# Kernel tuning notes

Hardware: AMD Instinct MI355X
Metric: run time of the kernel (lower is better)

## Reference

```python
import jax, jax.numpy as jnp
import numpy as np

# 4D conv dimension numbers: N=batch, C/I/O=channels, T,Z,Y,X = 4 spatial dims
DN = ('NCTZYX', 'OITZYX', 'NCTZYX')
PAD = [(1, 1)] * 4  # padding=1 on each of the 4 spatial dims


def setup_inputs() -> dict:
    key = jax.random.key(0)
    kx, kw = jax.random.split(key)
    B, Cin, Cout = 1, 16, 4
    T, D, H, Wd = 10, 32, 64, 64
    K = 3
    x = jax.random.normal(kx, (B, Cin, T, D, H, Wd), dtype=jnp.float32)
    # xavier_uniform over [Cout, Cin, 3,3,3,3]
    fan_in = Cin * K ** 4
    fan_out = Cout * K ** 4
    limit = float(np.sqrt(6.0 / (fan_in + fan_out)))
    W = jax.random.uniform(kw, (Cout, Cin, K, K, K, K), dtype=jnp.float32,
                           minval=-limit, maxval=limit)
    b = jnp.zeros((Cout,), dtype=jnp.float32)
    return {"x": x, "W": W, "b": b}


def reference(x, W, b):
    # True 4D convolution (stride 1, padding 1, 'same' output) + channel softmax
    y = jax.lax.conv_general_dilated(
        x, W,
        window_strides=(1, 1, 1, 1),
        padding=PAD,
        dimension_numbers=DN,
    )
    y = y + b[None, :, None, None, None, None]
    return jax.nn.softmax(y, axis=1)
```

## Files before the change

kernel.cpp:

```cpp
#include <hip/hip_runtime.h>
#include <hip/hip_bf16.h>

#define CIN  16
#define COUT 4
#define TT   10
#define ZZ   32
#define YY   64
#define XX   64

constexpr int SX_CI = TT * ZZ * YY * XX;
constexpr int SX_T  = ZZ * YY * XX;
constexpr int SX_Z  = YY * XX;
constexpr int WCO   = CIN * 81;

constexpr int XT_TB = ZZ * YY * XX * CIN * 2;
constexpr int XT_ZB = YY * XX * CIN * 2;
constexpr int XT_YB = XX * CIN * 2;
constexpr size_t XT_BYTES = (size_t)TT * XT_TB;
constexpr size_t BTAB     = XT_BYTES;
constexpr size_t ZOFF     = BTAB + 9 * 2048;
constexpr size_t WS_NEED  = ZOFF + 2048;

typedef short  short8 __attribute__((ext_vector_type(8)));
typedef float  f32x4  __attribute__((ext_vector_type(4)));

__device__ __forceinline__ unsigned short f2bf(float f) {
    union { __hip_bfloat16 h; unsigned short u; } c;
    c.h = __float2bfloat16(f);
    return c.u;
}
__device__ __forceinline__ unsigned int pk(float a, float b) {
    return (unsigned int)f2bf(a) | ((unsigned int)f2bf(b) << 16);
}

__global__ __launch_bounds__(256) void transpose_x(const float* __restrict__ x,
                                                   char* __restrict__ ws) {
    const int tid = threadIdx.x;
    const int wid = tid >> 6;
    const int i   = tid & 63;
    const int xp  = i >> 1;
    const int h   = i & 1;
    const int r   = blockIdx.x * 4 + wid;
    const int t   = r >> 11;
    const int rem = r & 2047;
    const int z   = rem >> 6;
    const int y   = rem & 63;
    const size_t base = (size_t)t * SX_T + (size_t)z * SX_Z +
                        (size_t)y * XX + 2 * xp;
    float2 v[8];
#pragma unroll
    for (int j = 0; j < 8; ++j)
        v[j] = *(const float2*)(x + (size_t)(h * 8 + j) * SX_CI + base);
    unsigned int w0[4], w1[4];
#pragma unroll
    for (int k = 0; k < 4; ++k) {
        w0[k] = pk(v[2 * k].x, v[2 * k + 1].x);
        w1[k] = pk(v[2 * k].y, v[2 * k + 1].y);
    }
    char* rowp = ws + (size_t)r * 2048 + xp * 64 + h * 16;
    *(uint4*)(rowp)      = make_uint4(w0[0], w0[1], w0[2], w0[3]);
    *(uint4*)(rowp + 32) = make_uint4(w1[0], w1[1], w1[2], w1[3]);
}

__global__ void prep_B(const float* __restrict__ W, char* __restrict__ ws) {
    const int g = blockIdx.x * 256 + threadIdx.x;
    if (g < 1152) {
        const int p = g >> 7, rem = g & 127, frag = rem >> 6, L = rem & 63;
        const int q = L >> 4, n = L & 15, co = n & 3, dx = n >> 2;
        const int dt = p / 3, dz = p % 3;
        unsigned int d[4];
#pragma unroll
        for (int j = 0; j < 4; ++j) {
            float v0 = 0.f, v1 = 0.f;
            if (dx < 3) {
                if (frag == 0) {
                    const int dy = q >> 1;
                    const int ci0 = (q & 1) * 8 + 2 * j;
                    v0 = W[(co * CIN + ci0) * 81 + dt * 27 + dz * 9 + dy * 3 + dx];
                    v1 = W[(co * CIN + ci0 + 1) * 81 + dt * 27 + dz * 9 + dy * 3 + dx];
                } else if (q < 2) {
                    const int ci0 = q * 8 + 2 * j;
                    v0 = W[(co * CIN + ci0) * 81 + dt * 27 + dz * 9 + 6 + dx];
                    v1 = W[(co * CIN + ci0 + 1) * 81 + dt * 27 + dz * 9 + 6 + dx];
                }
            }
            d[j] = pk(v0, v1);
        }
        *(uint4*)(ws + BTAB + (size_t)p * 2048 + frag * 1024 + (size_t)L * 16) =
            make_uint4(d[0], d[1], d[2], d[3]);
    } else if (g < 1280) {
        *(uint4*)(ws + ZOFF + (size_t)(g - 1152) * 16) = make_uint4(0, 0, 0, 0);
    }
}

#define GL16(SRC, DST) __builtin_amdgcn_global_load_lds( \
    (const __attribute__((address_space(1))) unsigned int*)(SRC), \
    (__attribute__((address_space(3))) unsigned int*)(DST), 16, 0, 0)

#define LROW 21
__global__ __launch_bounds__(256, 4) void conv_mfma(
        const char* __restrict__ ws,
        const float* __restrict__ bias,
        float* __restrict__ out) {
    __shared__ char smem[2 * 10 * 2048];
    const int lane = threadIdx.x;
    const int wid  = __builtin_amdgcn_readfirstlane(threadIdx.y);
    const int bid = blockIdx.x;
    const int xcd = bid & 7, lid = bid >> 3;
    const int z0 = 4 * xcd + 2 * (lid & 1);
    const int yq = (lid >> 1) & 7;
    const int t0 = lid >> 4;
    const int y0 = yq * 8;
    const int m = lane & 15, q = lane >> 4, h = q & 1, dyA = q >> 1;
    const int e2 = 2 * m + h;
    const int wid2 = wid * 2;

    f32x4 acc[2][2][4];
#pragma unroll
    for (int z = 0; z < 2; ++z)
#pragma unroll
        for (int r = 0; r < 2; ++r)
#pragma unroll
            for (int xt = 0; xt < 4; ++xt) acc[z][r][xt] = (f32x4){0.f, 0.f, 0.f, 0.f};

#define STAGE(P, BUF) { \
    constexpr int dtS = (P) >> 2, jS = (P) & 3; \
    const int t_in = t0 + dtS - 1, z_in = z0 + jS - 1; \
    const bool pv = ((unsigned)t_in < TT) && ((unsigned)z_in < ZZ); \
    const int pbase = pv ? (t_in * XT_TB + z_in * XT_ZB) : 0; \
    _Pragma("unroll") \
    for (int k = 0; k < 5; ++k) { \
        const int idx = wid + 4 * k; \
        const int rw = idx >> 1; \
        const int hf = (idx & 1) * 1024; \
        const int y_in = y0 - 1 + rw; \
        const bool rv = pv && ((unsigned)y_in < YY); \
        const char* srcS = ws + (rv ? (size_t)(pbase + y_in * XT_YB) : ZOFF) \
                              + hf + lane * 16; \
        GL16(srcS, smem + (BUF) * 20480 + rw * 2048 + hf + lane * 16); \
    } }

#define COMPUTE(P, BUF) { \
    constexpr int dtC = (P) >> 2, jC = (P) & 3; \
    constexpr int paC = dtC * 3 + (jC <= 2 ? jC : 0); \
    constexpr int pbC = dtC * 3 + (jC >= 1 ? jC - 1 : 0); \
    const char* bbC = smem + (BUF) * 20480; \
    const short8 BfAa = *(const short8*)(ws + BTAB + paC * 2048 + lane * 16); \
    const short8 BfBa = *(const short8*)(ws + BTAB + paC * 2048 + 1024 + lane * 16); \
    const short8 BfAb = *(const short8*)(ws + BTAB + pbC * 2048 + lane * 16); \
    const short8 BfBb = *(const short8*)(ws + BTAB + pbC * 2048 + 1024 + lane * 16); \
    _Pragma("unroll") \
    for (int xt = 0; xt < 4; ++xt) { \
        const int sw = (32 * xt + e2) * 16; \
        const char* colp = bbC + wid2 * 2048 + sw; \
        const short8 Rw0 = *(const short8*)(colp + 0 * 2048); \
        const short8 Rw1 = *(const short8*)(colp + 1 * 2048); \
        const short8 Rw2 = *(const short8*)(colp + 2 * 2048); \
        const short8 Rw3 = *(const short8*)(colp + 3 * 2048); \
        const short8 fa0 = dyA ? Rw1 : Rw0; \
        const short8 fa1 = dyA ? Rw2 : Rw1; \
        if (jC <= 2) { \
            acc[0][0][xt] = __builtin_amdgcn_mfma_f32_16x16x32_bf16(fa0, BfAa, acc[0][0][xt], 0, 0, 0); \
            acc[0][0][xt] = __builtin_amdgcn_mfma_f32_16x16x32_bf16(Rw2, BfBa, acc[0][0][xt], 0, 0, 0); \
            acc[0][1][xt] = __builtin_amdgcn_mfma_f32_16x16x32_bf16(fa1, BfAa, acc[0][1][xt], 0, 0, 0); \
            acc[0][1][xt] = __builtin_amdgcn_mfma_f32_16x16x32_bf16(Rw3, BfBa, acc[0][1][xt], 0, 0, 0); \
        } \
        if (jC >= 1) { \
            acc[1][0][xt] = __builtin_amdgcn_mfma_f32_16x16x32_bf16(fa0, BfAb, acc[1][0][xt], 0, 0, 0); \
            acc[1][0][xt] = __builtin_amdgcn_mfma_f32_16x16x32_bf16(Rw2, BfBb, acc[1][0][xt], 0, 0, 0); \
            acc[1][1][xt] = __builtin_amdgcn_mfma_f32_16x16x32_bf16(fa1, BfAb, acc[1][1][xt], 0, 0, 0); \
            acc[1][1][xt] = __builtin_amdgcn_mfma_f32_16x16x32_bf16(Rw3, BfBb, acc[1][1][xt], 0, 0, 0); \
        } \
    } }

    STAGE(0, 0)  __syncthreads();
    STAGE(1, 1)  COMPUTE(0, 0)  __syncthreads();
    STAGE(2, 0)  COMPUTE(1, 1)  __syncthreads();
    STAGE(3, 1)  COMPUTE(2, 0)  __syncthreads();
    STAGE(4, 0)  COMPUTE(3, 1)  __syncthreads();
    STAGE(5, 1)  COMPUTE(4, 0)  __syncthreads();
    STAGE(6, 0)  COMPUTE(5, 1)  __syncthreads();
    STAGE(7, 1)  COMPUTE(6, 0)  __syncthreads();
    STAGE(8, 0)  COMPUTE(7, 1)  __syncthreads();
    STAGE(9, 1)  COMPUTE(8, 0)  __syncthreads();
    STAGE(10, 0) COMPUTE(9, 1)  __syncthreads();
    STAGE(11, 1) COMPUTE(10, 0) __syncthreads();
    COMPUTE(11, 1) __syncthreads();
#undef STAGE
#undef COMPUTE

    const float bi0 = bias[0], bi1 = bias[1], bi2 = bias[2], bi3 = bias[3];
    float* swave = (float*)smem + wid * (66 * LROW);
    if (lane < LROW) {
        swave[lane] = 0.f;
        swave[65 * LROW + lane] = 0.f;
    }
    const int colw = lane & 15;
    const int rowq = (lane >> 4) * 4 + 1;
#pragma unroll
    for (int z = 0; z < 2; ++z) {
#pragma unroll
        for (int r = 0; r < 2; ++r) {
#pragma unroll
            for (int xt = 0; xt < 4; ++xt)
#pragma unroll
                for (int reg = 0; reg < 4; ++reg)
                    swave[(xt * 16 + rowq + reg) * LROW + colw] = acc[z][r][xt][reg];
            float lg0 = bi0, lg1 = bi1, lg2 = bi2, lg3 = bi3;
#pragma unroll
            for (int dx = 0; dx < 3; ++dx) {
                const float* sp = swave + (lane + dx) * LROW + dx * 4;
                lg0 += sp[0]; lg1 += sp[1]; lg2 += sp[2]; lg3 += sp[3];
            }
            const float mx = fmaxf(fmaxf(lg0, lg1), fmaxf(lg2, lg3));
            const float e0 = __expf(lg0 - mx);
            const float e1 = __expf(lg1 - mx);
            const float e2v = __expf(lg2 - mx);
            const float e3 = __expf(lg3 - mx);
            const float inv = 1.f / (e0 + e1 + e2v + e3);
            const int y = y0 + wid2 + r;
            float* op = out + (size_t)t0 * SX_T + (size_t)(z0 + z) * SX_Z +
                        (size_t)y * XX + lane;
            op[0 * (size_t)SX_CI] = e0 * inv;
            op[1 * (size_t)SX_CI] = e1 * inv;
            op[2 * (size_t)SX_CI] = e2v * inv;
            op[3 * (size_t)SX_CI] = e3 * inv;
        }
    }
}

__global__ __launch_bounds__(256, 4) void conv4d_softmax_vec(
        const float* __restrict__ x, const float* __restrict__ W,
        const float* __restrict__ b, float* __restrict__ out) {
    const int lane = threadIdx.x;
    const int xg = lane & 15, yl = lane >> 4;
    const int y = blockIdx.x * 16 + threadIdx.y * 4 + yl;
    const int z0 = blockIdx.y, t0 = blockIdx.z, x0 = xg * 4;
    float acc[COUT][4];
#pragma unroll
    for (int c = 0; c < COUT; ++c)
#pragma unroll
        for (int xi = 0; xi < 4; ++xi) acc[c][xi] = 0.f;
    for (int ci = 0; ci < CIN; ++ci) {
        const float* xc = x + (size_t)ci * SX_CI;
        const float* wc = W + ci * 81;
#pragma unroll
        for (int dt = 0; dt < 3; ++dt) {
            const int t_in = t0 + dt - 1;
            const int t_c = min(max(t_in, 0), TT - 1);
            const bool tv = (unsigned)t_in < TT;
#pragma unroll
            for (int dz = 0; dz < 3; ++dz) {
                const int z_in = z0 + dz - 1;
                const int z_c = min(max(z_in, 0), ZZ - 1);
                const bool tzvv = tv && ((unsigned)z_in < ZZ);
                const float* plane = xc + (size_t)t_c * SX_T + (size_t)z_c * SX_Z;
                const float* wb = wc + (dt * 3 + dz) * 9;
#pragma unroll
                for (int e = 0; e < 3; ++e) {
                    const int y_in = y + e - 1;
                    const int y_c = min(max(y_in, 0), YY - 1);
                    const bool v = tzvv && ((unsigned)y_in < YY);
                    float4 f = *(const float4*)(plane + y_c * XX + x0);
                    f.x = v ? f.x : 0.f; f.y = v ? f.y : 0.f;
                    f.z = v ? f.z : 0.f; f.w = v ? f.w : 0.f;
                    float hl = __shfl(f.w, (lane - 1) & 63, 64);
                    hl = (xg == 0) ? 0.f : hl;
                    float hr = __shfl(f.x, (lane + 1) & 63, 64);
                    hr = (xg == 15) ? 0.f : hr;
                    const float win[6] = {hl, f.x, f.y, f.z, f.w, hr};
#pragma unroll
                    for (int co = 0; co < COUT; ++co) {
                        const float* wp = wb + co * WCO + e * 3;
                        const float w0 = wp[0], w1 = wp[1], w2 = wp[2];
#pragma unroll
                        for (int xi = 0; xi < 4; ++xi) {
                            float a = acc[co][xi];
                            a = fmaf(win[xi], w0, a);
                            a = fmaf(win[xi + 1], w1, a);
                            a = fmaf(win[xi + 2], w2, a);
                            acc[co][xi] = a;
                        }
                    }
                }
            }
        }
    }
    const float b0 = b[0], b1 = b[1], b2 = b[2], b3 = b[3];
    float4 rr[COUT];
#pragma unroll
    for (int xi = 0; xi < 4; ++xi) {
        const float a0 = acc[0][xi] + b0, a1 = acc[1][xi] + b1;
        const float a2 = acc[2][xi] + b2, a3 = acc[3][xi] + b3;
        const float mm = fmaxf(fmaxf(a0, a1), fmaxf(a2, a3));
        const float e0 = __expf(a0 - mm), e1 = __expf(a1 - mm);
        const float e2 = __expf(a2 - mm), e3 = __expf(a3 - mm);
        const float inv = 1.f / (e0 + e1 + e2 + e3);
        ((float*)&rr[0])[xi] = e0 * inv; ((float*)&rr[1])[xi] = e1 * inv;
        ((float*)&rr[2])[xi] = e2 * inv; ((float*)&rr[3])[xi] = e3 * inv;
    }
    float* op = out + (size_t)t0 * SX_T + (size_t)z0 * SX_Z + (size_t)y * XX + x0;
#pragma unroll
    for (int co = 0; co < COUT; ++co)
        *(float4*)(op + (size_t)co * SX_CI) = rr[co];
}

extern "C" void kernel_launch(void* const* d_in, const int* in_sizes, int n_in,
                              void* d_out, int out_size, void* d_ws, size_t ws_size,
                              hipStream_t stream) {
    const float* x = (const float*)d_in[0];
    const float* W = (const float*)d_in[1];
    const float* b = (const float*)d_in[2];
    float* out = (float*)d_out;

    if (ws_size >= WS_NEED) {
        char* ws = (char*)d_ws;
        transpose_x<<<dim3(5120), dim3(256), 0, stream>>>(x, ws);
        prep_B<<<dim3(5), dim3(256), 0, stream>>>(W, ws);
        conv_mfma<<<dim3(1280), dim3(64, 4), 0, stream>>>(ws, b, out);
    } else {
        conv4d_softmax_vec<<<dim3(4, ZZ, TT), dim3(64, 4), 0, stream>>>(x, W, b, out);
    }
}
```

Baseline: 166.4 us.

## Triple-buffer conv staging, preload weights to registers, merge weight prep kernel

Moves the conv main loop from double to triple LDS buffering. It replaces __syncthreads with an explicit vmcnt wait plus a raw barrier, so two stages of global→LDS loads stay in flight while compute runs. All 9 weight-fragment pairs are preloaded into registers once, instead of being reloaded from global memory for every stage. The weight-prep kernel is folded into the transpose kernel as one extra block, which saves a launch. In exchange, the larger LDS footprint and extra registers lower occupancy (launch bounds drop from 4 to 2 blocks per CU), and the hand-written waitcnt must match the per-wave load count.

```diff
diff --git a/kernel.cpp b/kernel.cpp
--- a/kernel.cpp
+++ b/kernel.cpp
@@ -34,7 +34,42 @@
 }
 
 __global__ __launch_bounds__(256) void transpose_x(const float* __restrict__ x,
+                                                   const float* __restrict__ W,
                                                    char* __restrict__ ws) {
+    if (blockIdx.x >= 5120) {
+#pragma unroll
+        for (int it = 0; it < 5; ++it) {
+            const int g = it * 256 + threadIdx.x;
+            if (g < 1152) {
+                const int p = g >> 7, rem = g & 127, frag = rem >> 6, L = rem & 63;
+                const int q = L >> 4, n = L & 15, co = n & 3, dx = n >> 2;
+                const int dt = p / 3, dz = p % 3;
+                unsigned int d[4];
+#pragma unroll
+                for (int j = 0; j < 4; ++j) {
+                    float v0 = 0.f, v1 = 0.f;
+                    if (dx < 3) {
+                        if (frag == 0) {
+                            const int dy = q >> 1;
+                            const int ci0 = (q & 1) * 8 + 2 * j;
+                            v0 = W[(co * CIN + ci0) * 81 + dt * 27 + dz * 9 + dy * 3 + dx];
+                            v1 = W[(co * CIN + ci0 + 1) * 81 + dt * 27 + dz * 9 + dy * 3 + dx];
+                        } else if (q < 2) {
+                            const int ci0 = q * 8 + 2 * j;
+                            v0 = W[(co * CIN + ci0) * 81 + dt * 27 + dz * 9 + 6 + dx];
+                            v1 = W[(co * CIN + ci0 + 1) * 81 + dt * 27 + dz * 9 + 6 + dx];
+                        }
+                    }
+                    d[j] = pk(v0, v1);
+                }
+                *(uint4*)(ws + BTAB + (size_t)p * 2048 + frag * 1024 + (size_t)L * 16) =
+                    make_uint4(d[0], d[1], d[2], d[3]);
+            } else if (g < 1280) {
+                *(uint4*)(ws + ZOFF + (size_t)(g - 1152) * 16) = make_uint4(0, 0, 0, 0);
+            }
+        }
+        return;
+    }
     const int tid = threadIdx.x;
     const int wid = tid >> 6;
     const int i   = tid & 63;
@@ -62,47 +97,19 @@
     *(uint4*)(rowp + 32) = make_uint4(w1[0], w1[1], w1[2], w1[3]);
 }
 
-__global__ void prep_B(const float* __restrict__ W, char* __restrict__ ws) {
-    const int g = blockIdx.x * 256 + threadIdx.x;
-    if (g < 1152) {
-        const int p = g >> 7, rem = g & 127, frag = rem >> 6, L = rem & 63;
-        const int q = L >> 4, n = L & 15, co = n & 3, dx = n >> 2;
-        const int dt = p / 3, dz = p % 3;
-        unsigned int d[4];
-#pragma unroll
-        for (int j = 0; j < 4; ++j) {
-            float v0 = 0.f, v1 = 0.f;
-            if (dx < 3) {
-                if (frag == 0) {
-                    const int dy = q >> 1;
-                    const int ci0 = (q & 1) * 8 + 2 * j;
-                    v0 = W[(co * CIN + ci0) * 81 + dt * 27 + dz * 9 + dy * 3 + dx];
-                    v1 = W[(co * CIN + ci0 + 1) * 81 + dt * 27 + dz * 9 + dy * 3 + dx];
-                } else if (q < 2) {
-                    const int ci0 = q * 8 + 2 * j;
-                    v0 = W[(co * CIN + ci0) * 81 + dt * 27 + dz * 9 + 6 + dx];
-                    v1 = W[(co * CIN + ci0 + 1) * 81 + dt * 27 + dz * 9 + 6 + dx];
-                }
-            }
-            d[j] = pk(v0, v1);
-        }
-        *(uint4*)(ws + BTAB + (size_t)p * 2048 + frag * 1024 + (size_t)L * 16) =
-            make_uint4(d[0], d[1], d[2], d[3]);
-    } else if (g < 1280) {
-        *(uint4*)(ws + ZOFF + (size_t)(g - 1152) * 16) = make_uint4(0, 0, 0, 0);
-    }
-}
-
 #define GL16(SRC, DST) __builtin_amdgcn_global_load_lds( \
     (const __attribute__((address_space(1))) unsigned int*)(SRC), \
     (__attribute__((address_space(3))) unsigned int*)(DST), 16, 0, 0)
 
+#define VMCNT(N) asm volatile("s_waitcnt vmcnt(" #N ")" ::: "memory")
+#define RBAR()   { __builtin_amdgcn_s_barrier(); asm volatile("" ::: "memory"); }
+
 #define LROW 21
-__global__ __launch_bounds__(256, 4) void conv_mfma(
+__global__ __launch_bounds__(256, 2) void conv_mfma(
         const char* __restrict__ ws,
         const float* __restrict__ bias,
         float* __restrict__ out) {
-    __shared__ char smem[2 * 10 * 2048];
+    __shared__ char smem[3 * 10 * 2048];
     const int lane = threadIdx.x;
     const int wid  = __builtin_amdgcn_readfirstlane(threadIdx.y);
     const int bid = blockIdx.x;
@@ -114,6 +121,13 @@
     const int m = lane & 15, q = lane >> 4, h = q & 1, dyA = q >> 1;
     const int e2 = 2 * m + h;
     const int wid2 = wid * 2;
+
+    short8 BF[9][2];
+#pragma unroll
+    for (int pp = 0; pp < 9; ++pp) {
+        BF[pp][0] = *(const short8*)(ws + BTAB + (size_t)pp * 2048 + lane * 16);
+        BF[pp][1] = *(const short8*)(ws + BTAB + (size_t)pp * 2048 + 1024 + lane * 16);
+    }
 
     f32x4 acc[2][2][4];
 #pragma unroll
@@ -145,10 +159,6 @@
     constexpr int paC = dtC * 3 + (jC <= 2 ? jC : 0); \
     constexpr int pbC = dtC * 3 + (jC >= 1 ? jC - 1 : 0); \
     const char* bbC = smem + (BUF) * 20480; \
-    const short8 BfAa = *(const short8*)(ws + BTAB + paC * 2048 + lane * 16); \
-    const short8 BfBa = *(const short8*)(ws + BTAB + paC * 2048 + 1024 + lane * 16); \
-    const short8 BfAb = *(const short8*)(ws + BTAB + pbC * 2048 + lane * 16); \
-    const short8 BfBb = *(const short8*)(ws + BTAB + pbC * 2048 + 1024 + lane * 16); \
     _Pragma("unroll") \
     for (int xt = 0; xt < 4; ++xt) { \
         const int sw = (32 * xt + e2) * 16; \
@@ -160,34 +170,35 @@
         const short8 fa0 = dyA ? Rw1 : Rw0; \
         const short8 fa1 = dyA ? Rw2 : Rw1; \
         if (jC <= 2) { \
-            acc[0][0][xt] = __builtin_amdgcn_mfma_f32_16x16x32_bf16(fa0, BfAa, acc[0][0][xt], 0, 0, 0); \
-            acc[0][0][xt] = __builtin_amdgcn_mfma_f32_16x16x32_bf16(Rw2, BfBa, acc[0][0][xt], 0, 0, 0); \
-            acc[0][1][xt] = __builtin_amdgcn_mfma_f32_16x16x32_bf16(fa1, BfAa, acc[0][1][xt], 0, 0, 0); \
-            acc[0][1][xt] = __builtin_amdgcn_mfma_f32_16x16x32_bf16(Rw3, BfBa, acc[0][1][xt], 0, 0, 0); \
+            acc[0][0][xt] = __builtin_amdgcn_mfma_f32_16x16x32_bf16(fa0, BF[paC][0], acc[0][0][xt], 0, 0, 0); \
+            acc[0][0][xt] = __builtin_amdgcn_mfma_f32_16x16x32_bf16(Rw2, BF[paC][1], acc[0][0][xt], 0, 0, 0); \
+            acc[0][1][xt] = __builtin_amdgcn_mfma_f32_16x16x32_bf16(fa1, BF[paC][0], acc[0][1][xt], 0, 0, 0); \
+            acc[0][1][xt] = __builtin_amdgcn_mfma_f32_16x16x32_bf16(Rw3, BF[paC][1], acc[0][1][xt], 0, 0, 0); \
         } \
         if (jC >= 1) { \
-            acc[1][0][xt] = __builtin_amdgcn_mfma_f32_16x16x32_bf16(fa0, BfAb, acc[1][0][xt], 0, 0, 0); \
-            acc[1][0][xt] = __builtin_amdgcn_mfma_f32_16x16x32_bf16(Rw2, BfBb, acc[1][0][xt], 0, 0, 0); \
-            acc[1][1][xt] = __builtin_amdgcn_mfma_f32_16x16x32_bf16(fa1, BfAb, acc[1][1][xt], 0, 0, 0); \
-            acc[1][1][xt] = __builtin_amdgcn_mfma_f32_16x16x32_bf16(Rw3, BfBb, acc[1][1][xt], 0, 0, 0); \
+            acc[1][0][xt] = __builtin_amdgcn_mfma_f32_16x16x32_bf16(fa0, BF[pbC][0], acc[1][0][xt], 0, 0, 0); \
+            acc[1][0][xt] = __builtin_amdgcn_mfma_f32_16x16x32_bf16(Rw2, BF[pbC][1], acc[1][0][xt], 0, 0, 0); \
+            acc[1][1][xt] = __builtin_amdgcn_mfma_f32_16x16x32_bf16(fa1, BF[pbC][0], acc[1][1][xt], 0, 0, 0); \
+            acc[1][1][xt] = __builtin_amdgcn_mfma_f32_16x16x32_bf16(Rw3, BF[pbC][1], acc[1][1][xt], 0, 0, 0); \
         } \
     } }
 
-    STAGE(0, 0)  __syncthreads();
-    STAGE(1, 1)  COMPUTE(0, 0)  __syncthreads();
-    STAGE(2, 0)  COMPUTE(1, 1)  __syncthreads();
-    STAGE(3, 1)  COMPUTE(2, 0)  __syncthreads();
-    STAGE(4, 0)  COMPUTE(3, 1)  __syncthreads();
-    STAGE(5, 1)  COMPUTE(4, 0)  __syncthreads();
-    STAGE(6, 0)  COMPUTE(5, 1)  __syncthreads();
-    STAGE(7, 1)  COMPUTE(6, 0)  __syncthreads();
-    STAGE(8, 0)  COMPUTE(7, 1)  __syncthreads();
-    STAGE(9, 1)  COMPUTE(8, 0)  __syncthreads();
-    STAGE(10, 0) COMPUTE(9, 1)  __syncthreads();
-    STAGE(11, 1) COMPUTE(10, 0) __syncthreads();
-    COMPUTE(11, 1) __syncthreads();
+    STAGE(0, 0) STAGE(1, 1)
+    VMCNT(5);  RBAR();  COMPUTE(0, 0)   STAGE(2, 2)
+    VMCNT(5);  RBAR();  COMPUTE(1, 1)   STAGE(3, 0)
+    VMCNT(5);  RBAR();  COMPUTE(2, 2)   STAGE(4, 1)
+    VMCNT(5);  RBAR();  COMPUTE(3, 0)   STAGE(5, 2)
+    VMCNT(5);  RBAR();  COMPUTE(4, 1)   STAGE(6, 0)
+    VMCNT(5);  RBAR();  COMPUTE(5, 2)   STAGE(7, 1)
+    VMCNT(5);  RBAR();  COMPUTE(6, 0)   STAGE(8, 2)
+    VMCNT(5);  RBAR();  COMPUTE(7, 1)   STAGE(9, 0)
+    VMCNT(5);  RBAR();  COMPUTE(8, 2)   STAGE(10, 1)
+    VMCNT(5);  RBAR();  COMPUTE(9, 0)   STAGE(11, 2)
+    VMCNT(5);  RBAR();  COMPUTE(10, 1)
+    VMCNT(0);  RBAR();  COMPUTE(11, 2)
 #undef STAGE
 #undef COMPUTE
+    __syncthreads();
 
     const float bi0 = bias[0], bi1 = bias[1], bi2 = bias[2], bi3 = bias[3];
     float* swave = (float*)smem + wid * (66 * LROW);
@@ -315,8 +326,7 @@
 
     if (ws_size >= WS_NEED) {
         char* ws = (char*)d_ws;
-        transpose_x<<<dim3(5120), dim3(256), 0, stream>>>(x, ws);
-        prep_B<<<dim3(5), dim3(256), 0, stream>>>(W, ws);
+        transpose_x<<<dim3(5121), dim3(256), 0, stream>>>(x, W, ws);
         conv_mfma<<<dim3(1280), dim3(64, 4), 0, stream>>>(ws, b, out);
     } else {
         conv4d_softmax_vec<<<dim3(4, ZZ, TT), dim3(64, 4), 0, stream>>>(x, W, b, out);
```

Result: no change. 167.9 us (+0.8%).

## Fuse input transpose and weight prep into single MFMA conv kernel

Applied to the files above, without the earlier changes.

Removes the separate transpose_x and prep_B kernels and the workspace round trip. Each block now loads fp32 input rows directly, converts them to bf16 in the channel-interleaved layout, and writes them into shared memory in its staging step. Weight fragments are built in registers at kernel start. This saves two launches and the global write and re-read of the transposed tensor. The cost is synchronous loads in place of async global_load_lds, redundant halo conversion across blocks, and higher register pressure, with launch bounds lowered from 4 to 2 blocks per CU.

```diff
diff --git a/kernel.cpp b/kernel.cpp
--- a/kernel.cpp
+++ b/kernel.cpp
@@ -11,15 +11,6 @@
 constexpr int SX_CI = TT * ZZ * YY * XX;
 constexpr int SX_T  = ZZ * YY * XX;
 constexpr int SX_Z  = YY * XX;
-constexpr int WCO   = CIN * 81;
-
-constexpr int XT_TB = ZZ * YY * XX * CIN * 2;
-constexpr int XT_ZB = YY * XX * CIN * 2;
-constexpr int XT_YB = XX * CIN * 2;
-constexpr size_t XT_BYTES = (size_t)TT * XT_TB;
-constexpr size_t BTAB     = XT_BYTES;
-constexpr size_t ZOFF     = BTAB + 9 * 2048;
-constexpr size_t WS_NEED  = ZOFF + 2048;
 
 typedef short  short8 __attribute__((ext_vector_type(8)));
 typedef float  f32x4  __attribute__((ext_vector_type(4)));
@@ -33,73 +24,10 @@
     return (unsigned int)f2bf(a) | ((unsigned int)f2bf(b) << 16);
 }
 
-__global__ __launch_bounds__(256) void transpose_x(const float* __restrict__ x,
-                                                   char* __restrict__ ws) {
-    const int tid = threadIdx.x;
-    const int wid = tid >> 6;
-    const int i   = tid & 63;
-    const int xp  = i >> 1;
-    const int h   = i & 1;
-    const int r   = blockIdx.x * 4 + wid;
-    const int t   = r >> 11;
-    const int rem = r & 2047;
-    const int z   = rem >> 6;
-    const int y   = rem & 63;
-    const size_t base = (size_t)t * SX_T + (size_t)z * SX_Z +
-                        (size_t)y * XX + 2 * xp;
-    float2 v[8];
-#pragma unroll
-    for (int j = 0; j < 8; ++j)
-        v[j] = *(const float2*)(x + (size_t)(h * 8 + j) * SX_CI + base);
-    unsigned int w0[4], w1[4];
-#pragma unroll
-    for (int k = 0; k < 4; ++k) {
-        w0[k] = pk(v[2 * k].x, v[2 * k + 1].x);
-        w1[k] = pk(v[2 * k].y, v[2 * k + 1].y);
-    }
-    char* rowp = ws + (size_t)r * 2048 + xp * 64 + h * 16;
-    *(uint4*)(rowp)      = make_uint4(w0[0], w0[1], w0[2], w0[3]);
-    *(uint4*)(rowp + 32) = make_uint4(w1[0], w1[1], w1[2], w1[3]);
-}
-
-__global__ void prep_B(const float* __restrict__ W, char* __restrict__ ws) {
-    const int g = blockIdx.x * 256 + threadIdx.x;
-    if (g < 1152) {
-        const int p = g >> 7, rem = g & 127, frag = rem >> 6, L = rem & 63;
-        const int q = L >> 4, n = L & 15, co = n & 3, dx = n >> 2;
-        const int dt = p / 3, dz = p % 3;
-        unsigned int d[4];
-#pragma unroll
-        for (int j = 0; j < 4; ++j) {
-            float v0 = 0.f, v1 = 0.f;
-            if (dx < 3) {
-                if (frag == 0) {
-                    const int dy = q >> 1;
-                    const int ci0 = (q & 1) * 8 + 2 * j;
-                    v0 = W[(co * CIN + ci0) * 81 + dt * 27 + dz * 9 + dy * 3 + dx];
-                    v1 = W[(co * CIN + ci0 + 1) * 81 + dt * 27 + dz * 9 + dy * 3 + dx];
-                } else if (q < 2) {
-                    const int ci0 = q * 8 + 2 * j;
-                    v0 = W[(co * CIN + ci0) * 81 + dt * 27 + dz * 9 + 6 + dx];
-                    v1 = W[(co * CIN + ci0 + 1) * 81 + dt * 27 + dz * 9 + 6 + dx];
-                }
-            }
-            d[j] = pk(v0, v1);
-        }
-        *(uint4*)(ws + BTAB + (size_t)p * 2048 + frag * 1024 + (size_t)L * 16) =
-            make_uint4(d[0], d[1], d[2], d[3]);
-    } else if (g < 1280) {
-        *(uint4*)(ws + ZOFF + (size_t)(g - 1152) * 16) = make_uint4(0, 0, 0, 0);
-    }
-}
-
-#define GL16(SRC, DST) __builtin_amdgcn_global_load_lds( \
-    (const __attribute__((address_space(1))) unsigned int*)(SRC), \
-    (__attribute__((address_space(3))) unsigned int*)(DST), 16, 0, 0)
-
 #define LROW 21
-__global__ __launch_bounds__(256, 4) void conv_mfma(
-        const char* __restrict__ ws,
+__global__ __launch_bounds__(256, 2) void conv_fused(
+        const float* __restrict__ x,
+        const float* __restrict__ W,
         const float* __restrict__ bias,
         float* __restrict__ out) {
     __shared__ char smem[2 * 10 * 2048];
@@ -114,6 +42,38 @@
     const int m = lane & 15, q = lane >> 4, h = q & 1, dyA = q >> 1;
     const int e2 = 2 * m + h;
     const int wid2 = wid * 2;
+    const int xp = lane >> 1;
+    const int hs = lane & 1;
+
+    short8 BF[9][2];
+    {
+        const int n = lane & 15, qq = lane >> 4;
+        const int co = n & 3, dx = n >> 2;
+#pragma unroll
+        for (int pp = 0; pp < 9; ++pp) {
+            const int dt = pp / 3, dz = pp % 3;
+            union { unsigned u[4]; short8 s; } u0, u1;
+#pragma unroll
+            for (int j = 0; j < 4; ++j) {
+                float a0 = 0.f, a1 = 0.f, b0 = 0.f, b1 = 0.f;
+                if (dx < 3) {
+                    const int dy = qq >> 1;
+                    const int ci0 = (qq & 1) * 8 + 2 * j;
+                    a0 = W[(co * CIN + ci0) * 81 + dt * 27 + dz * 9 + dy * 3 + dx];
+                    a1 = W[(co * CIN + ci0 + 1) * 81 + dt * 27 + dz * 9 + dy * 3 + dx];
+                    if (qq < 2) {
+                        const int cj0 = qq * 8 + 2 * j;
+                        b0 = W[(co * CIN + cj0) * 81 + dt * 27 + dz * 9 + 6 + dx];
+                        b1 = W[(co * CIN + cj0 + 1) * 81 + dt * 27 + dz * 9 + 6 + dx];
+                    }
+                }
+                u0.u[j] = pk(a0, a1);
+                u1.u[j] = pk(b0, b1);
+            }
+            BF[pp][0] = u0.s;
+            BF[pp][1] = u1.s;
+        }
+    }
 
     f32x4 acc[2][2][4];
 #pragma unroll
@@ -127,17 +87,32 @@
     constexpr int dtS = (P) >> 2, jS = (P) & 3; \
     const int t_in = t0 + dtS - 1, z_in = z0 + jS - 1; \
     const bool pv = ((unsigned)t_in < TT) && ((unsigned)z_in < ZZ); \
-    const int pbase = pv ? (t_in * XT_TB + z_in * XT_ZB) : 0; \
+    const int tc = min(max(t_in, 0), TT - 1), zc = min(max(z_in, 0), ZZ - 1); \
+    const float* pb = x + (size_t)tc * SX_T + (size_t)zc * SX_Z + 2 * xp; \
     _Pragma("unroll") \
-    for (int k = 0; k < 5; ++k) { \
-        const int idx = wid + 4 * k; \
-        const int rw = idx >> 1; \
-        const int hf = (idx & 1) * 1024; \
-        const int y_in = y0 - 1 + rw; \
+    for (int rr = wid; rr < 10; rr += 4) { \
+        const int y_in = y0 - 1 + rr; \
         const bool rv = pv && ((unsigned)y_in < YY); \
-        const char* srcS = ws + (rv ? (size_t)(pbase + y_in * XT_YB) : ZOFF) \
-                              + hf + lane * 16; \
-        GL16(srcS, smem + (BUF) * 20480 + rw * 2048 + hf + lane * 16); \
+        const int yc = min(max(y_in, 0), YY - 1); \
+        const float* rp = pb + yc * XX; \
+        float2 v[8]; \
+        if (rv) { \
+            _Pragma("unroll") \
+            for (int j = 0; j < 8; ++j) \
+                v[j] = *(const float2*)(rp + (size_t)(hs * 8 + j) * SX_CI); \
+        } else { \
+            _Pragma("unroll") \
+            for (int j = 0; j < 8; ++j) v[j] = make_float2(0.f, 0.f); \
+        } \
+        unsigned w0[4], w1[4]; \
+        _Pragma("unroll") \
+        for (int k = 0; k < 4; ++k) { \
+            w0[k] = pk(v[2 * k].x, v[2 * k + 1].x); \
+            w1[k] = pk(v[2 * k].y, v[2 * k + 1].y); \
+        } \
+        char* dp = smem + (BUF) * 20480 + rr * 2048 + xp * 64 + hs * 16; \
+        *(uint4*)(dp)      = make_uint4(w0[0], w0[1], w0[2], w0[3]); \
+        *(uint4*)(dp + 32) = make_uint4(w1[0], w1[1], w1[2], w1[3]); \
     } }
 
 #define COMPUTE(P, BUF) { \
@@ -145,10 +120,6 @@
     constexpr int paC = dtC * 3 + (jC <= 2 ? jC : 0); \
     constexpr int pbC = dtC * 3 + (jC >= 1 ? jC - 1 : 0); \
     const char* bbC = smem + (BUF) * 20480; \
-    const short8 BfAa = *(const short8*)(ws + BTAB + paC * 2048 + lane * 16); \
-    const short8 BfBa = *(const short8*)(ws + BTAB + paC * 2048 + 1024 + lane * 16); \
-    const short8 BfAb = *(const short8*)(ws + BTAB + pbC * 2048 + lane * 16); \
-    const short8 BfBb = *(const short8*)(ws + BTAB + pbC * 2048 + 1024 + lane * 16); \
     _Pragma("unroll") \
     for (int xt = 0; xt < 4; ++xt) { \
         const int sw = (32 * xt + e2) * 16; \
@@ -160,16 +131,16 @@
         const short8 fa0 = dyA ? Rw1 : Rw0; \
         const short8 fa1 = dyA ? Rw2 : Rw1; \
         if (jC <= 2) { \
-            acc[0][0][xt] = __builtin_amdgcn_mfma_f32_16x16x32_bf16(fa0, BfAa, acc[0][0][xt], 0, 0, 0); \
-            acc[0][0][xt] = __builtin_amdgcn_mfma_f32_16x16x32_bf16(Rw2, BfBa, acc[0][0][xt], 0, 0, 0); \
-            acc[0][1][xt] = __builtin_amdgcn_mfma_f32_16x16x32_bf16(fa1, BfAa, acc[0][1][xt], 0, 0, 0); \
-            acc[0][1][xt] = __builtin_amdgcn_mfma_f32_16x16x32_bf16(Rw3, BfBa, acc[0][1][xt], 0, 0, 0); \
+            acc[0][0][xt] = __builtin_amdgcn_mfma_f32_16x16x32_bf16(fa0, BF[paC][0], acc[0][0][xt], 0, 0, 0); \
+            acc[0][0][xt] = __builtin_amdgcn_mfma_f32_16x16x32_bf16(Rw2, BF[paC][1], acc[0][0][xt], 0, 0, 0); \
+            acc[0][1][xt] = __builtin_amdgcn_mfma_f32_16x16x32_bf16(fa1, BF[paC][0], acc[0][1][xt], 0, 0, 0); \
+            acc[0][1][xt] = __builtin_amdgcn_mfma_f32_16x16x32_bf16(Rw3, BF[paC][1], acc[0][1][xt], 0, 0, 0); \
         } \
         if (jC >= 1) { \
-            acc[1][0][xt] = __builtin_amdgcn_mfma_f32_16x16x32_bf16(fa0, BfAb, acc[1][0][xt], 0, 0, 0); \
-            acc[1][0][xt] = __builtin_amdgcn_mfma_f32_16x16x32_bf16(Rw2, BfBb, acc[1][0][xt], 0, 0, 0); \
-            acc[1][1][xt] = __builtin_amdgcn_mfma_f32_16x16x32_bf16(fa1, BfAb, acc[1][1][xt], 0, 0, 0); \
-            acc[1][1][xt] = __builtin_amdgcn_mfma_f32_16x16x32_bf16(Rw3, BfBb, acc[1][1][xt], 0, 0, 0); \
+            acc[1][0][xt] = __builtin_amdgcn_mfma_f32_16x16x32_bf16(fa0, BF[pbC][0], acc[1][0][xt], 0, 0, 0); \
+            acc[1][0][xt] = __builtin_amdgcn_mfma_f32_16x16x32_bf16(Rw2, BF[pbC][1], acc[1][0][xt], 0, 0, 0); \
+            acc[1][1][xt] = __builtin_amdgcn_mfma_f32_16x16x32_bf16(fa1, BF[pbC][0], acc[1][1][xt], 0, 0, 0); \
+            acc[1][1][xt] = __builtin_amdgcn_mfma_f32_16x16x32_bf16(Rw3, BF[pbC][1], acc[1][1][xt], 0, 0, 0); \
         } \
     } }
 
@@ -229,82 +200,6 @@
     }
 }
 
-__global__ __launch_bounds__(256, 4) void conv4d_softmax_vec(
-        const float* __restrict__ x, const float* __restrict__ W,
-        const float* __restrict__ b, float* __restrict__ out) {
-    const int lane = threadIdx.x;
-    const int xg = lane & 15, yl = lane >> 4;
-    const int y = blockIdx.x * 16 + threadIdx.y * 4 + yl;
-    const int z0 = blockIdx.y, t0 = blockIdx.z, x0 = xg * 4;
-    float acc[COUT][4];
-#pragma unroll
-    for (int c = 0; c < COUT; ++c)
-#pragma unroll
-        for (int xi = 0; xi < 4; ++xi) acc[c][xi] = 0.f;
-    for (int ci = 0; ci < CIN; ++ci) {
-        const float* xc = x + (size_t)ci * SX_CI;
-        const float* wc = W + ci * 81;
-#pragma unroll
-        for (int dt = 0; dt < 3; ++dt) {
-            const int t_in = t0 + dt - 1;
-            const int t_c = min(max(t_in, 0), TT - 1);
-            const bool tv = (unsigned)t_in < TT;
-#pragma unroll
-            for (int dz = 0; dz < 3; ++dz) {
-                const int z_in = z0 + dz - 1;
-                const int z_c = min(max(z_in, 0), ZZ - 1);
-                const bool tzvv = tv && ((unsigned)z_in < ZZ);
-                const float* plane = xc + (size_t)t_c * SX_T + (size_t)z_c * SX_Z;
-                const float* wb = wc + (dt * 3 + dz) * 9;
-#pragma unroll
-                for (int e = 0; e < 3; ++e) {
-                    const int y_in = y + e - 1;
-                    const int y_c = min(max(y_in, 0), YY - 1);
-                    const bool v = tzvv && ((unsigned)y_in < YY);
-                    float4 f = *(const float4*)(plane + y_c * XX + x0);
-                    f.x = v ? f.x : 0.f; f.y = v ? f.y : 0.f;
-                    f.z = v ? f.z : 0.f; f.w = v ? f.w : 0.f;
-                    float hl = __shfl(f.w, (lane - 1) & 63, 64);
-                    hl = (xg == 0) ? 0.f : hl;
-                    float hr = __shfl(f.x, (lane + 1) & 63, 64);
-                    hr = (xg == 15) ? 0.f : hr;
-                    const float win[6] = {hl, f.x, f.y, f.z, f.w, hr};
-#pragma unroll
-                    for (int co = 0; co < COUT; ++co) {
-                        const float* wp = wb + co * WCO + e * 3;
-                        const float w0 = wp[0], w1 = wp[1], w2 = wp[2];
-#pragma unroll
-                        for (int xi = 0; xi < 4; ++xi) {
-                            float a = acc[co][xi];
-                            a = fmaf(win[xi], w0, a);
-                            a = fmaf(win[xi + 1], w1, a);
-                            a = fmaf(win[xi + 2], w2, a);
-                            acc[co][xi] = a;
-                        }
-                    }
-                }
-            }
-        }
-    }
-    const float b0 = b[0], b1 = b[1], b2 = b[2], b3 = b[3];
-    float4 rr[COUT];
-#pragma unroll
-    for (int xi = 0; xi < 4; ++xi) {
-        const float a0 = acc[0][xi] + b0, a1 = acc[1][xi] + b1;
-        const float a2 = acc[2][xi] + b2, a3 = acc[3][xi] + b3;
-        const float mm = fmaxf(fmaxf(a0, a1), fmaxf(a2, a3));
-        const float e0 = __expf(a0 - mm), e1 = __expf(a1 - mm);
-        const float e2 = __expf(a2 - mm), e3 = __expf(a3 - mm);
-        const float inv = 1.f / (e0 + e1 + e2 + e3);
-        ((float*)&rr[0])[xi] = e0 * inv; ((float*)&rr[1])[xi] = e1 * inv;
-        ((float*)&rr[2])[xi] = e2 * inv; ((float*)&rr[3])[xi] = e3 * inv;
-    }
-    float* op = out + (size_t)t0 * SX_T + (size_t)z0 * SX_Z + (size_t)y * XX + x0;
-#pragma unroll
-    for (int co = 0; co < COUT; ++co)
-        *(float4*)(op + (size_t)co * SX_CI) = rr[co];
-}
-
 extern "C" void kernel_launch(void* const* d_in, const int* in_sizes, int n_in,
                               void* d_out, int out_size, void* d_ws, size_t ws_size,
                               hipStream_t stream) {
@@ -312,13 +207,6 @@
     const float* W = (const float*)d_in[1];
     const float* b = (const float*)d_in[2];
     float* out = (float*)d_out;
-
-    if (ws_size >= WS_NEED) {
-        char* ws = (char*)d_ws;
-        transpose_x<<<dim3(5120), dim3(256), 0, stream>>>(x, ws);
-        prep_B<<<dim3(5), dim3(256), 0, stream>>>(W, ws);
-        conv_mfma<<<dim3(1280), dim3(64, 4), 0, stream>>>(ws, b, out);
-    } else {
-        conv4d_softmax_vec<<<dim3(4, ZZ, TT), dim3(64, 4), 0, stream>>>(x, W, b, out);
-    }
-}
+    (void)d_ws; (void)ws_size;
+    conv_fused<<<dim3(1280), dim3(64, 4), 0, stream>>>(x, W, b, out);
+}
```

Result: slower. 239.3 us (+43.8%).
